# Optimization experiments

Hardware: AMD Instinct MI355X
Metric: run time of the kernel (lower is better)

The kernel has to match this reference:

```python
import jax, jax.numpy as jnp
import numpy as np
import math

L = 4      # model_layers
D = 512    # model_filters
H = 32     # heads = max(D//16, 1)
DH = D // H  # 16
S = 1024   # dataset_dimension == max_len == seq_len
B = 2
EPS = 1e-5


def setup_inputs() -> dict:
    key = jax.random.key(0)
    ks = jax.random.split(key, 12)
    scale = 0.02
    n = lambda k, shape: jax.random.normal(k, shape, dtype=jnp.float32) * scale
    return {
        "x": jax.random.normal(ks[0], (B, S), dtype=jnp.float32),
        "Winit": n(ks[1], (D,)),               # init_linear weight (1->D)
        "binit": jnp.zeros((D,), jnp.float32),
        "Wq": n(ks[2], (L, D, D)), "bq": jnp.zeros((L, D), jnp.float32),
        "Wk": n(ks[3], (L, D, D)), "bk": jnp.zeros((L, D), jnp.float32),
        "Wv": n(ks[4], (L, D, D)), "bv": jnp.zeros((L, D), jnp.float32),
        "Er": jax.random.normal(ks[5], (L, S, DH), dtype=jnp.float32) * scale,
        "Wlin": n(ks[6], (L, D, D)), "blin": jnp.zeros((L, D), jnp.float32),
        "ln_g": jnp.ones((L, D), jnp.float32), "ln_b": jnp.zeros((L, D), jnp.float32),
        "Wout": n(ks[7], (D, 1)),              # output_linear, no bias
    }


def layernorm(x, g, b):
    mu = jnp.mean(x, axis=-1, keepdims=True)
    var = jnp.mean(jnp.square(x - mu), axis=-1, keepdims=True)
    return (x - mu) * jax.lax.rsqrt(var + EPS) * g + b


def rel_attn(h, Wq, bq, Wk, bk, Wv, bv, Er):
    # h: [B, S, D]
    b_, s_, _ = h.shape
    q = (h @ Wq + bq).reshape(b_, s_, H, DH).transpose(0, 2, 1, 3)  # [B,H,S,dh]
    k = (h @ Wk + bk).reshape(b_, s_, H, DH).transpose(0, 2, 1, 3)
    v = (h @ Wv + bv).reshape(b_, s_, H, DH).transpose(0, 2, 1, 3)
    # relative-position term with skew trick (seq_len == max_len -> full Er)
    QEr = jnp.einsum('bhsd,td->bhst', q, Er)                  # [B,H,S,S]
    padded = jnp.pad(QEr, ((0, 0), (0, 0), (0, 0), (1, 0)))   # pad left of last dim
    Srel = padded.reshape(b_, H, s_ + 1, s_)[:, :, 1:, :]     # skew
    scores = (jnp.einsum('bhsd,bhtd->bhst', q, k) + Srel) / math.sqrt(DH)
    mask = jnp.tril(jnp.ones((s_, s_), dtype=bool))           # causal
    scores = jnp.where(mask, scores, -jnp.inf)
    p = jax.nn.softmax(scores, axis=-1)
    o = jnp.einsum('bhst,bhtd->bhsd', p, v)
    return o.transpose(0, 2, 1, 3).reshape(b_, s_, D)


def reference(x, Winit, binit, Wq, bq, Wk, bk, Wv, bv, Er, Wlin, blin, ln_g, ln_b, Wout):
    # init_linear(1->D) on scalar per position, then exact gelu
    h = jax.nn.gelu(x[..., None] * Winit + binit, approximate=False)  # [B,S,D]
    for l in range(L):
        a = rel_attn(h, Wq[l], bq[l], Wk[l], bk[l], Wv[l], bv[l], Er[l])
        y = layernorm(a @ Wlin[l] + blin[l], ln_g[l], ln_b[l])
        h = h + jax.nn.gelu(y, approximate=False)
    return h.sum(axis=-2) @ Wout  # [B,1]
```

## Files before the change

kernel.cpp:

```cpp
#include <hip/hip_runtime.h>
#include <math.h>

#define NL 4
#define DIM 512
#define NH 32
#define DHD 16
#define SEQ 1024
#define NB 2
#define LN_EPS 1e-5f
#define NEGF (-1e30f)
#define QSC 0.36067376022224085f

typedef _Float16 half4 __attribute__((ext_vector_type(4)));
typedef _Float16 half8 __attribute__((ext_vector_type(8)));
typedef float floatx4 __attribute__((ext_vector_type(4)));

__device__ __forceinline__ float gelu_exact(float x) {
    return 0.5f * x * (1.0f + erff(x * 0.70710678118654752f));
}

__device__ __forceinline__ void async16(const void* g, void* l) {
    __builtin_amdgcn_global_load_lds(
        (const __attribute__((address_space(1))) void*)g,
        (__attribute__((address_space(3))) void*)l, 16, 0, 0);
}

__global__ __launch_bounds__(256) void k_prep_all(const float* __restrict__ Wq,
        const float* __restrict__ Wk, const float* __restrict__ Wv,
        const float* __restrict__ Wlin, const float* __restrict__ bq,
        const float* __restrict__ bk, const float* __restrict__ bv,
        const float* __restrict__ Er, const float* __restrict__ x,
        const float* __restrict__ Wi, const float* __restrict__ bi,
        _Float16* __restrict__ Wqkvt, _Float16* __restrict__ Wlint,
        float* __restrict__ bqkv, _Float16* __restrict__ Erh,
        float* __restrict__ h, _Float16* __restrict__ hf) {
    __shared__ _Float16 lt[64][72];
    const int u = blockIdx.x;
    const int tid = threadIdx.x;
    if (u < 1024) {
        const int kx = u & 7, ny = (u >> 3) & 7, mz = u >> 6;
        const int l = mz >> 2, which = mz & 3;
        const float* src = (which == 0) ? Wq : (which == 1) ? Wk : (which == 2) ? Wv : Wlin;
        src += (size_t)l * 262144;
        const float scale = (which == 0) ? QSC : 1.0f;
        _Float16* dst = (which < 3) ? (Wqkvt + (size_t)l * 786432 + (size_t)which * 262144)
                                    : (Wlint + (size_t)l * 262144);
        const int k0 = kx << 6, n0 = ny << 6;
        #pragma unroll
        for (int p = 0; p < 4; p++) {
            int kl = (p << 4) + (tid >> 4);
            int n4 = (tid & 15) << 2;
            float4 wv = *(const float4*)(src + (size_t)(k0 + kl) * 512 + n0 + n4);
            lt[n4 + 0][kl] = (_Float16)(wv.x * scale);
            lt[n4 + 1][kl] = (_Float16)(wv.y * scale);
            lt[n4 + 2][kl] = (_Float16)(wv.z * scale);
            lt[n4 + 3][kl] = (_Float16)(wv.w * scale);
        }
        __syncthreads();
        int nl = tid >> 2, k16 = (tid & 3) << 4;
        float4* d4 = (float4*)(dst + (size_t)(n0 + nl) * 512 + k0 + k16);
        const float4* s4 = (const float4*)&lt[nl][k16];
        d4[0] = s4[0];
        d4[1] = s4[1];
    } else if (u < 2048) {
        int idx0 = ((u - 1024) << 10) + (tid << 2);
        int d = idx0 & 511, bs = idx0 >> 9;
        float xs = x[bs];
        float4 wv = *(const float4*)(Wi + d);
        float4 bv = *(const float4*)(bi + d);
        float4 r;
        r.x = gelu_exact(xs * wv.x + bv.x);
        r.y = gelu_exact(xs * wv.y + bv.y);
        r.z = gelu_exact(xs * wv.z + bv.z);
        r.w = gelu_exact(xs * wv.w + bv.w);
        *(float4*)(h + idx0) = r;
        half4 rh = {(_Float16)r.x, (_Float16)r.y, (_Float16)r.z, (_Float16)r.w};
        *(half4*)(hf + idx0) = rh;
    } else {
        int idx = ((u - 2048) << 8) + tid;
        if (idx < NL * 1536) {
            int l = idx / 1536, j = idx % 1536;
            int which = j >> 9, jj = j & 511;
            float val = (which == 0) ? bq[l * 512 + jj] * QSC
                      : (which == 1) ? bk[l * 512 + jj] : bv[l * 512 + jj];
            bqkv[idx] = val;
        }
        int e = idx - NL * 1536;
        if (e >= 0 && e < NL * SEQ * DHD) Erh[e] = (_Float16)Er[e];
    }
}

__global__ __launch_bounds__(256) void k_gemm_qkv(const _Float16* __restrict__ A,
        const _Float16* __restrict__ Bt, const float* __restrict__ bias,
        _Float16* __restrict__ o16) {
    __shared__ _Float16 As[2 * 64 * 32];
    __shared__ _Float16 Bs[2 * 128 * 32];
    const int tid = threadIdx.x;
    const int w = tid >> 6, lane = tid & 63;
    const int nn = lane & 15, qd = lane >> 4;
    const int wm = (w & 1) << 5, wn = (w >> 1) << 6;
    const int m0 = blockIdx.x << 6, n0 = blockIdx.y << 7;
    const int l2r = lane >> 2, l2c = (lane & 3) << 3;
    const _Float16* Ag = A + (size_t)(m0 + (w << 4) + l2r) * 512 + l2c;
    const _Float16* Bg = Bt + (size_t)(n0 + (w << 5) + l2r) * 512 + l2c;
    _Float16* Al = As + (w << 9);
    _Float16* Bl = Bs + (w << 10);
    floatx4 acc[2][4] = {};
    for (int k0 = 0; k0 < 512; k0 += 64) {
        __syncthreads();
        #pragma unroll
        for (int p = 0; p < 2; p++) {
            async16(Ag + k0 + (p << 5), Al + (p << 11));
            async16(Bg + k0 + (p << 5), Bl + (p << 12));
            async16(Bg + k0 + (p << 5) + (16 << 9), Bl + (p << 12) + (16 << 5));
        }
        __syncthreads();
        #pragma unroll
        for (int ks = 0; ks < 2; ks++) {
            half8 af[2], bf[4];
            #pragma unroll
            for (int t = 0; t < 2; t++)
                af[t] = *(const half8*)&As[(ks << 11) + ((wm + (t << 4) + nn) << 5) + (qd << 3)];
            #pragma unroll
            for (int t = 0; t < 4; t++)
                bf[t] = *(const half8*)&Bs[(ks << 12) + ((wn + (t << 4) + nn) << 5) + (qd << 3)];
            #pragma unroll
            for (int ti = 0; ti < 2; ti++)
                #pragma unroll
                for (int tj = 0; tj < 4; tj++)
                    acc[ti][tj] = __builtin_amdgcn_mfma_f32_16x16x32_f16(
                            af[ti], bf[tj], acc[ti][tj], 0, 0, 0);
        }
    }
    float bv4[4];
    #pragma unroll
    for (int tj = 0; tj < 4; tj++) bv4[tj] = bias[n0 + wn + (tj << 4) + nn];
    #pragma unroll
    for (int ti = 0; ti < 2; ti++) {
        int rowg = m0 + wm + (ti << 4) + (qd << 2);
        #pragma unroll
        for (int tj = 0; tj < 4; tj++) {
            int colg = n0 + wn + (tj << 4) + nn;
            int which = colg >> 9, ci = colg & 511;
            _Float16* op = o16 + (size_t)which * 1048576 + (size_t)rowg * 512 + ci;
            #pragma unroll
            for (int r = 0; r < 4; r++)
                op[(size_t)r * 512] = (_Float16)(acc[ti][tj][r] + bv4[tj]);
        }
    }
}

__global__ __launch_bounds__(256) void k_gemm_lin(const _Float16* __restrict__ A,
        const _Float16* __restrict__ Bt, const float* __restrict__ bias,
        float* __restrict__ y) {
    __shared__ _Float16 As[2 * 64 * 32];
    __shared__ _Float16 Bs[2 * 64 * 32];
    const int tid = threadIdx.x;
    const int w = tid >> 6, lane = tid & 63;
    const int nn = lane & 15, qd = lane >> 4;
    const int wm = (w & 1) << 5, wn = (w >> 1) << 5;
    const int m0 = blockIdx.x << 6, n0 = blockIdx.y << 6;
    const int l2r = lane >> 2, l2c = (lane & 3) << 3;
    const _Float16* Ag = A + (size_t)(m0 + (w << 4) + l2r) * 512 + l2c;
    const _Float16* Bg = Bt + (size_t)(n0 + (w << 4) + l2r) * 512 + l2c;
    _Float16* Al = As + (w << 9);
    _Float16* Bl = Bs + (w << 9);
    floatx4 acc[2][2] = {};
    for (int k0 = 0; k0 < 512; k0 += 64) {
        __syncthreads();
        #pragma unroll
        for (int p = 0; p < 2; p++) {
            async16(Ag + k0 + (p << 5), Al + (p << 11));
            async16(Bg + k0 + (p << 5), Bl + (p << 11));
        }
        __syncthreads();
        #pragma unroll
        for (int ks = 0; ks < 2; ks++) {
            half8 af[2], bf[2];
            #pragma unroll
            for (int t = 0; t < 2; t++) {
                af[t] = *(const half8*)&As[(ks << 11) + ((wm + (t << 4) + nn) << 5) + (qd << 3)];
                bf[t] = *(const half8*)&Bs[(ks << 11) + ((wn + (t << 4) + nn) << 5) + (qd << 3)];
            }
            #pragma unroll
            for (int ti = 0; ti < 2; ti++)
                #pragma unroll
                for (int tj = 0; tj < 2; tj++)
                    acc[ti][tj] = __builtin_amdgcn_mfma_f32_16x16x32_f16(
                            af[ti], bf[tj], acc[ti][tj], 0, 0, 0);
        }
    }
    float bv2[2];
    #pragma unroll
    for (int tj = 0; tj < 2; tj++) bv2[tj] = bias[n0 + wn + (tj << 4) + nn];
    #pragma unroll
    for (int ti = 0; ti < 2; ti++) {
        int rg = m0 + wm + (ti << 4) + (qd << 2);
        #pragma unroll
        for (int tj = 0; tj < 2; tj++) {
            int colg = n0 + wn + (tj << 4) + nn;
            float* op = y + (size_t)rg * 512 + colg;
            #pragma unroll
            for (int r = 0; r < 4; r++)
                op[(size_t)r * 512] = acc[ti][tj][r] + bv2[tj];
        }
    }
}

__global__ __launch_bounds__(256, 4) void k_attn_mfma(const _Float16* __restrict__ q,
        const _Float16* __restrict__ k, const _Float16* __restrict__ v,
        const _Float16* __restrict__ Er, _Float16* __restrict__ aout) {
    __shared__ _Float16 Ks[256][20];
    __shared__ _Float16 Vts[16][268];
    __shared__ float Rel[4][16][80];
    const int tid = threadIdx.x;
    const int wid = tid >> 6, lane = tid & 63;
    const int nn = lane & 15, a4 = (lane >> 4) << 2;
    const int b_ = blockIdx.x >> 5, h_ = blockIdx.x & 31;
    const int y = blockIdx.y;
    const int t_ = tid >> 2, c4 = (tid & 3) << 2;
    const int r0p[2] = {64 * y, 64 * (15 - y)};
    const int R = r0p[1] + 64;

    half4 qf[2];
    floatx4 O[2];
    float m[2], lsum[2];
    #pragma unroll
    for (int ph = 0; ph < 2; ph++) {
        int s0w = r0p[ph] + (wid << 4);
        qf[ph] = *(const half4*)(q + ((size_t)(b_ * SEQ + s0w + nn)) * DIM + h_ * DHD + a4);
        O[ph] = (floatx4){0.f, 0.f, 0.f, 0.f};
        m[ph] = NEGF;
        lsum[ph] = 0.f;
    }

    for (int part = 0; part < 4; part++) {
        const int p0 = part << 8;
        if (p0 >= R) break;
        const int pend = (R < p0 + 256) ? R : (p0 + 256);
        __syncthreads();
        const int ng = (pend - p0) >> 6;
        for (int g = 0; g < ng; g++) {
            int rl = (g << 6) + t_;
            size_t gb = ((size_t)(b_ * SEQ + p0 + rl)) * DIM + h_ * DHD + c4;
            *(half4*)&Ks[rl][c4] = *(const half4*)(k + gb);
            half4 vv4 = *(const half4*)(v + gb);
            Vts[c4 + 0][rl] = vv4.x;
            Vts[c4 + 1][rl] = vv4.y;
            Vts[c4 + 2][rl] = vv4.z;
            Vts[c4 + 3][rl] = vv4.w;
        }
        __syncthreads();
        #pragma unroll
        for (int ph = 0; ph < 2; ph++) {
            const int r0 = r0p[ph];
            const int s0w = r0 + (wid << 4);
            const int hi = (r0 + 64 < pend) ? (r0 + 64) : pend;
            for (int ct = p0; ct < hi; ct += 64) {
                const int ctl = ct - p0;
                const int jbw = 1008 - s0w + ct;
                #pragma unroll
                for (int jt = 0; jt < 5; jt++) {
                    int j = jbw + (jt << 4) + nn;
                    j = (j < SEQ - 1) ? j : (SEQ - 1);
                    half4 ef = *(const half4*)(Er + (size_t)j * DHD + a4);
                    floatx4 racc = {0.f, 0.f, 0.f, 0.f};
                    racc = __builtin_amdgcn_mfma_f32_16x16x16f16(ef, qf[ph], racc, 0, 0, 0);
                    *(floatx4*)&Rel[wid][nn][(jt << 4) + a4] = racc;
                }
                float st[4][4];
                const bool diag = (ct == r0);
                #pragma unroll
                for (int tt = 0; tt < 4; tt++) {
                    half4 kf = *(const half4*)&Ks[ctl + (tt << 4) + nn][a4];
                    floatx4 sacc = {0.f, 0.f, 0.f, 0.f};
                    sacc = __builtin_amdgcn_mfma_f32_16x16x16f16(kf, qf[ph], sacc, 0, 0, 0);
                    #pragma unroll
                    for (int r = 0; r < 4; r++) {
                        int tl = (tt << 4) + a4 + r;
                        float sv = sacc[r] + Rel[wid][nn][15 - nn + tl];
                        if (diag && (tl > (wid << 4) + nn)) sv = NEGF;
                        st[tt][r] = sv;
                    }
                }
                float cmax = NEGF;
                #pragma unroll
                for (int tt = 0; tt < 4; tt++)
                    #pragma unroll
                    for (int r = 0; r < 4; r++) cmax = fmaxf(cmax, st[tt][r]);
                cmax = fmaxf(cmax, __shfl_xor(cmax, 16));
                cmax = fmaxf(cmax, __shfl_xor(cmax, 32));
                float mnew = fmaxf(m[ph], cmax);
                float alpha = exp2f(m[ph] - mnew);
                m[ph] = mnew;
                float csum = 0.f;
                half4 pf[4];
                #pragma unroll
                for (int tt = 0; tt < 4; tt++) {
                    float p0e = exp2f(st[tt][0] - mnew);
                    float p1e = exp2f(st[tt][1] - mnew);
                    float p2e = exp2f(st[tt][2] - mnew);
                    float p3e = exp2f(st[tt][3] - mnew);
                    csum += (p0e + p1e) + (p2e + p3e);
                    half4 ph4 = {(_Float16)p0e, (_Float16)p1e, (_Float16)p2e, (_Float16)p3e};
                    pf[tt] = ph4;
                }
                lsum[ph] = lsum[ph] * alpha + csum;
                O[ph][0] *= alpha; O[ph][1] *= alpha; O[ph][2] *= alpha; O[ph][3] *= alpha;
                #pragma unroll
                for (int tt = 0; tt < 4; tt++) {
                    half4 vf = *(const half4*)&Vts[nn][ctl + (tt << 4) + a4];
                    O[ph] = __builtin_amdgcn_mfma_f32_16x16x16f16(vf, pf[tt], O[ph], 0, 0, 0);
                }
            }
        }
    }
    #pragma unroll
    for (int ph = 0; ph < 2; ph++) {
        float lt = lsum[ph];
        lt += __shfl_xor(lt, 16);
        lt += __shfl_xor(lt, 32);
        float linv = 1.0f / lt;
        int s0w = r0p[ph] + (wid << 4);
        half4 ov = { (_Float16)(O[ph][0] * linv), (_Float16)(O[ph][1] * linv),
                     (_Float16)(O[ph][2] * linv), (_Float16)(O[ph][3] * linv) };
        *(half4*)(aout + ((size_t)(b_ * SEQ + s0w + nn)) * DIM + h_ * DHD + a4) = ov;
    }
}

__global__ __launch_bounds__(256) void k_ln_gelu_res(const float* __restrict__ y,
        const float* __restrict__ gam, const float* __restrict__ bet,
        float* __restrict__ h, _Float16* __restrict__ hf) {
    int row = (blockIdx.x << 2) + (threadIdx.x >> 6);
    int lane = threadIdx.x & 63;
    const float* yr = y + (size_t)row * DIM + (lane << 3);
    float4 v0 = *(const float4*)(yr);
    float4 v1 = *(const float4*)(yr + 4);
    float sum = (v0.x + v0.y) + (v0.z + v0.w) + (v1.x + v1.y) + (v1.z + v1.w);
    float sq = v0.x*v0.x + v0.y*v0.y + v0.z*v0.z + v0.w*v0.w
             + v1.x*v1.x + v1.y*v1.y + v1.z*v1.z + v1.w*v1.w;
    #pragma unroll
    for (int off = 32; off > 0; off >>= 1) {
        sum += __shfl_xor(sum, off);
        sq  += __shfl_xor(sq, off);
    }
    float mu = sum * (1.0f / DIM);
    float var = sq * (1.0f / DIM) - mu * mu;
    float rs = rsqrtf(var + LN_EPS);
    float4 g0 = *(const float4*)(gam + (lane << 3));
    float4 g1 = *(const float4*)(gam + (lane << 3) + 4);
    float4 b0 = *(const float4*)(bet + (lane << 3));
    float4 b1 = *(const float4*)(bet + (lane << 3) + 4);
    float* hr = h + (size_t)row * DIM + (lane << 3);
    float4 h0 = *(const float4*)(hr);
    float4 h1 = *(const float4*)(hr + 4);
    float o[8];
    o[0] = h0.x + gelu_exact((v0.x - mu) * rs * g0.x + b0.x);
    o[1] = h0.y + gelu_exact((v0.y - mu) * rs * g0.y + b0.y);
    o[2] = h0.z + gelu_exact((v0.z - mu) * rs * g0.z + b0.z);
    o[3] = h0.w + gelu_exact((v0.w - mu) * rs * g0.w + b0.w);
    o[4] = h1.x + gelu_exact((v1.x - mu) * rs * g1.x + b1.x);
    o[5] = h1.y + gelu_exact((v1.y - mu) * rs * g1.y + b1.y);
    o[6] = h1.z + gelu_exact((v1.z - mu) * rs * g1.z + b1.z);
    o[7] = h1.w + gelu_exact((v1.w - mu) * rs * g1.w + b1.w);
    *(float4*)(hr)     = make_float4(o[0], o[1], o[2], o[3]);
    *(float4*)(hr + 4) = make_float4(o[4], o[5], o[6], o[7]);
    half8 oh = {(_Float16)o[0], (_Float16)o[1], (_Float16)o[2], (_Float16)o[3],
                (_Float16)o[4], (_Float16)o[5], (_Float16)o[6], (_Float16)o[7]};
    *(half8*)(hf + (size_t)row * DIM + (lane << 3)) = oh;
}

__global__ __launch_bounds__(256) void k_colsum(const float* __restrict__ h,
        float* __restrict__ partial) {
    int bt = blockIdx.x;
    int b_ = bt >> 4, t = bt & 15;
    int tid = threadIdx.x;
    #pragma unroll
    for (int half = 0; half < 2; half++) {
        int d = half * 256 + tid;
        float acc = 0.f;
        for (int i = 0; i < 64; i++)
            acc += h[((size_t)(b_ * SEQ + t * 64 + i)) * DIM + d];
        partial[(size_t)bt * DIM + d] = acc;
    }
}

__global__ __launch_bounds__(256) void k_final(const float* __restrict__ partial,
        const float* __restrict__ Wout, float* __restrict__ out) {
    __shared__ float red[4][2];
    int tid = threadIdx.x;
    float acc0 = 0.f, acc1 = 0.f;
    #pragma unroll
    for (int half = 0; half < 2; half++) {
        int d = half * 256 + tid;
        float w = Wout[d];
        float s0 = 0.f, s1 = 0.f;
        for (int t = 0; t < 16; t++) {
            s0 += partial[t * DIM + d];
            s1 += partial[(16 + t) * DIM + d];
        }
        acc0 += s0 * w;
        acc1 += s1 * w;
    }
    #pragma unroll
    for (int off = 32; off > 0; off >>= 1) {
        acc0 += __shfl_down(acc0, off);
        acc1 += __shfl_down(acc1, off);
    }
    if ((tid & 63) == 0) { red[tid >> 6][0] = acc0; red[tid >> 6][1] = acc1; }
    __syncthreads();
    if (tid == 0) {
        out[0] = red[0][0] + red[1][0] + red[2][0] + red[3][0];
        out[1] = red[0][1] + red[1][1] + red[2][1] + red[3][1];
    }
}

extern "C" void kernel_launch(void* const* d_in, const int* in_sizes, int n_in,
                              void* d_out, int out_size, void* d_ws, size_t ws_size,
                              hipStream_t stream) {
    const float* x    = (const float*)d_in[0];
    const float* Wi   = (const float*)d_in[1];
    const float* bi   = (const float*)d_in[2];
    const float* Wq   = (const float*)d_in[3];
    const float* bq   = (const float*)d_in[4];
    const float* Wk   = (const float*)d_in[5];
    const float* bk   = (const float*)d_in[6];
    const float* Wv   = (const float*)d_in[7];
    const float* bv   = (const float*)d_in[8];
    const float* Er   = (const float*)d_in[9];
    const float* Wlin = (const float*)d_in[10];
    const float* blin = (const float*)d_in[11];
    const float* lng  = (const float*)d_in[12];
    const float* lnb  = (const float*)d_in[13];
    const float* Wout = (const float*)d_in[14];
    float* out = (float*)d_out;

    float* ws = (float*)d_ws;
    const size_t N1 = 1048576;
    float*     h     = ws;
    _Float16*  hf    = (_Float16*)(ws + N1);
    _Float16*  qh    = (_Float16*)(ws + N1 + N1/2);
    _Float16*  ah    = (_Float16*)(ws + 3 * N1);
    float*     y     = ws + 3 * N1 + N1/2;
    _Float16*  Wqkvt = (_Float16*)(ws + 4 * N1 + N1/2);
    _Float16*  Wlint = (_Float16*)(ws + 6 * N1);
    float*     bqkv  = ws + 6 * N1 + N1/2;
    _Float16*  Erh   = (_Float16*)(ws + 6 * N1 + N1/2 + 8192);
    float*     pa    = ws + 6 * N1 + N1/2 + 8192 + 32768;

    k_prep_all<<<dim3(2328), dim3(256), 0, stream>>>(Wq, Wk, Wv, Wlin, bq, bk, bv,
            Er, x, Wi, bi, Wqkvt, Wlint, bqkv, Erh, h, hf);
    for (int l = 0; l < NL; l++) {
        k_gemm_qkv<<<dim3(32, 12), dim3(256), 0, stream>>>(
                hf, Wqkvt + (size_t)l * 786432, bqkv + l * 1536, qh);
        k_attn_mfma<<<dim3(NB * NH, 8), dim3(256), 0, stream>>>(
                qh, qh + 1048576, qh + 2097152, Erh + (size_t)l * 16384, ah);
        k_gemm_lin<<<dim3(32, 8), dim3(256), 0, stream>>>(
                ah, Wlint + (size_t)l * 262144, blin + l * 512, y);
        k_ln_gelu_res<<<dim3(512), dim3(256), 0, stream>>>(
                y, lng + l * 512, lnb + l * 512, h, hf);
    }
    k_colsum<<<dim3(32), dim3(256), 0, stream>>>(h, pa);
    k_final<<<dim3(1), dim3(256), 0, stream>>>(pa, Wout, out);
}
```

Baseline: 315.0 us.

## Split attention into one row tile per block and shrink QKV GEMM tiles

The attention kernel no longer pairs a low and a high 64-row tile per block to balance causal work. Each block now handles one 64-row query tile, so the grid grows to 16 tiles per head and gets more parallelism and fewer live registers, at the cost of uneven per-block work. The QKV GEMM now reuses the 64x64-tile linear GEMM as a template, doubling its grid to 768 blocks at the cost of reloading each A tile more often.

```diff
diff --git a/kernel.cpp b/kernel.cpp
--- a/kernel.cpp
+++ b/kernel.cpp
@@ -90,69 +90,10 @@
     }
 }
 
-__global__ __launch_bounds__(256) void k_gemm_qkv(const _Float16* __restrict__ A,
+template<int F16OUT>
+__global__ __launch_bounds__(256) void k_gemm(const _Float16* __restrict__ A,
         const _Float16* __restrict__ Bt, const float* __restrict__ bias,
-        _Float16* __restrict__ o16) {
-    __shared__ _Float16 As[2 * 64 * 32];
-    __shared__ _Float16 Bs[2 * 128 * 32];
-    const int tid = threadIdx.x;
-    const int w = tid >> 6, lane = tid & 63;
-    const int nn = lane & 15, qd = lane >> 4;
-    const int wm = (w & 1) << 5, wn = (w >> 1) << 6;
-    const int m0 = blockIdx.x << 6, n0 = blockIdx.y << 7;
-    const int l2r = lane >> 2, l2c = (lane & 3) << 3;
-    const _Float16* Ag = A + (size_t)(m0 + (w << 4) + l2r) * 512 + l2c;
-    const _Float16* Bg = Bt + (size_t)(n0 + (w << 5) + l2r) * 512 + l2c;
-    _Float16* Al = As + (w << 9);
-    _Float16* Bl = Bs + (w << 10);
-    floatx4 acc[2][4] = {};
-    for (int k0 = 0; k0 < 512; k0 += 64) {
-        __syncthreads();
-        #pragma unroll
-        for (int p = 0; p < 2; p++) {
-            async16(Ag + k0 + (p << 5), Al + (p << 11));
-            async16(Bg + k0 + (p << 5), Bl + (p << 12));
-            async16(Bg + k0 + (p << 5) + (16 << 9), Bl + (p << 12) + (16 << 5));
-        }
-        __syncthreads();
-        #pragma unroll
-        for (int ks = 0; ks < 2; ks++) {
-            half8 af[2], bf[4];
-            #pragma unroll
-            for (int t = 0; t < 2; t++)
-                af[t] = *(const half8*)&As[(ks << 11) + ((wm + (t << 4) + nn) << 5) + (qd << 3)];
-            #pragma unroll
-            for (int t = 0; t < 4; t++)
-                bf[t] = *(const half8*)&Bs[(ks << 12) + ((wn + (t << 4) + nn) << 5) + (qd << 3)];
-            #pragma unroll
-            for (int ti = 0; ti < 2; ti++)
-                #pragma unroll
-                for (int tj = 0; tj < 4; tj++)
-                    acc[ti][tj] = __builtin_amdgcn_mfma_f32_16x16x32_f16(
-                            af[ti], bf[tj], acc[ti][tj], 0, 0, 0);
-        }
-    }
-    float bv4[4];
-    #pragma unroll
-    for (int tj = 0; tj < 4; tj++) bv4[tj] = bias[n0 + wn + (tj << 4) + nn];
-    #pragma unroll
-    for (int ti = 0; ti < 2; ti++) {
-        int rowg = m0 + wm + (ti << 4) + (qd << 2);
-        #pragma unroll
-        for (int tj = 0; tj < 4; tj++) {
-            int colg = n0 + wn + (tj << 4) + nn;
-            int which = colg >> 9, ci = colg & 511;
-            _Float16* op = o16 + (size_t)which * 1048576 + (size_t)rowg * 512 + ci;
-            #pragma unroll
-            for (int r = 0; r < 4; r++)
-                op[(size_t)r * 512] = (_Float16)(acc[ti][tj][r] + bv4[tj]);
-        }
-    }
-}
-
-__global__ __launch_bounds__(256) void k_gemm_lin(const _Float16* __restrict__ A,
-        const _Float16* __restrict__ Bt, const float* __restrict__ bias,
-        float* __restrict__ y) {
+        _Float16* __restrict__ o16, float* __restrict__ o32) {
     __shared__ _Float16 As[2 * 64 * 32];
     __shared__ _Float16 Bs[2 * 64 * 32];
     const int tid = threadIdx.x;
@@ -199,10 +140,18 @@
         #pragma unroll
         for (int tj = 0; tj < 2; tj++) {
             int colg = n0 + wn + (tj << 4) + nn;
-            float* op = y + (size_t)rg * 512 + colg;
-            #pragma unroll
-            for (int r = 0; r < 4; r++)
-                op[(size_t)r * 512] = acc[ti][tj][r] + bv2[tj];
+            if (F16OUT) {
+                int which = colg >> 9, ci = colg & 511;
+                _Float16* op = o16 + (size_t)which * 1048576 + (size_t)rg * 512 + ci;
+                #pragma unroll
+                for (int r = 0; r < 4; r++)
+                    op[(size_t)r * 512] = (_Float16)(acc[ti][tj][r] + bv2[tj]);
+            } else {
+                float* op = o32 + (size_t)rg * 512 + colg;
+                #pragma unroll
+                for (int r = 0; r < 4; r++)
+                    op[(size_t)r * 512] = acc[ti][tj][r] + bv2[tj];
+            }
         }
     }
 }
@@ -219,20 +168,13 @@
     const int b_ = blockIdx.x >> 5, h_ = blockIdx.x & 31;
     const int y = blockIdx.y;
     const int t_ = tid >> 2, c4 = (tid & 3) << 2;
-    const int r0p[2] = {64 * y, 64 * (15 - y)};
-    const int R = r0p[1] + 64;
-
-    half4 qf[2];
-    floatx4 O[2];
-    float m[2], lsum[2];
-    #pragma unroll
-    for (int ph = 0; ph < 2; ph++) {
-        int s0w = r0p[ph] + (wid << 4);
-        qf[ph] = *(const half4*)(q + ((size_t)(b_ * SEQ + s0w + nn)) * DIM + h_ * DHD + a4);
-        O[ph] = (floatx4){0.f, 0.f, 0.f, 0.f};
-        m[ph] = NEGF;
-        lsum[ph] = 0.f;
-    }
+    const int r0 = y << 6;
+    const int s0w = r0 + (wid << 4);
+    const int R = r0 + 64;
+
+    half4 qf = *(const half4*)(q + ((size_t)(b_ * SEQ + s0w + nn)) * DIM + h_ * DHD + a4);
+    floatx4 O = {0.f, 0.f, 0.f, 0.f};
+    float m = NEGF, lsum = 0.f;
 
     for (int part = 0; part < 4; part++) {
         const int p0 = part << 8;
@@ -251,81 +193,71 @@
             Vts[c4 + 3][rl] = vv4.w;
         }
         __syncthreads();
-        #pragma unroll
-        for (int ph = 0; ph < 2; ph++) {
-            const int r0 = r0p[ph];
-            const int s0w = r0 + (wid << 4);
-            const int hi = (r0 + 64 < pend) ? (r0 + 64) : pend;
-            for (int ct = p0; ct < hi; ct += 64) {
-                const int ctl = ct - p0;
-                const int jbw = 1008 - s0w + ct;
-                #pragma unroll
-                for (int jt = 0; jt < 5; jt++) {
-                    int j = jbw + (jt << 4) + nn;
-                    j = (j < SEQ - 1) ? j : (SEQ - 1);
-                    half4 ef = *(const half4*)(Er + (size_t)j * DHD + a4);
-                    floatx4 racc = {0.f, 0.f, 0.f, 0.f};
-                    racc = __builtin_amdgcn_mfma_f32_16x16x16f16(ef, qf[ph], racc, 0, 0, 0);
-                    *(floatx4*)&Rel[wid][nn][(jt << 4) + a4] = racc;
+        for (int ct = p0; ct < pend; ct += 64) {
+            const int ctl = ct - p0;
+            const int jbw = 1008 - s0w + ct;
+            #pragma unroll
+            for (int jt = 0; jt < 5; jt++) {
+                int j = jbw + (jt << 4) + nn;
+                j = (j < SEQ - 1) ? j : (SEQ - 1);
+                half4 ef = *(const half4*)(Er + (size_t)j * DHD + a4);
+                floatx4 racc = {0.f, 0.f, 0.f, 0.f};
+                racc = __builtin_amdgcn_mfma_f32_16x16x16f16(ef, qf, racc, 0, 0, 0);
+                *(floatx4*)&Rel[wid][nn][(jt << 4) + a4] = racc;
+            }
+            float st[4][4];
+            const bool diag = (ct == r0);
+            #pragma unroll
+            for (int tt = 0; tt < 4; tt++) {
+                half4 kf = *(const half4*)&Ks[ctl + (tt << 4) + nn][a4];
+                floatx4 sacc = {0.f, 0.f, 0.f, 0.f};
+                sacc = __builtin_amdgcn_mfma_f32_16x16x16f16(kf, qf, sacc, 0, 0, 0);
+                #pragma unroll
+                for (int r = 0; r < 4; r++) {
+                    int tl = (tt << 4) + a4 + r;
+                    float sv = sacc[r] + Rel[wid][nn][15 - nn + tl];
+                    if (diag && (tl > (wid << 4) + nn)) sv = NEGF;
+                    st[tt][r] = sv;
                 }
-                float st[4][4];
-                const bool diag = (ct == r0);
-                #pragma unroll
-                for (int tt = 0; tt < 4; tt++) {
-                    half4 kf = *(const half4*)&Ks[ctl + (tt << 4) + nn][a4];
-                    floatx4 sacc = {0.f, 0.f, 0.f, 0.f};
-                    sacc = __builtin_amdgcn_mfma_f32_16x16x16f16(kf, qf[ph], sacc, 0, 0, 0);
-                    #pragma unroll
-                    for (int r = 0; r < 4; r++) {
-                        int tl = (tt << 4) + a4 + r;
-                        float sv = sacc[r] + Rel[wid][nn][15 - nn + tl];
-                        if (diag && (tl > (wid << 4) + nn)) sv = NEGF;
-                        st[tt][r] = sv;
-                    }
-                }
-                float cmax = NEGF;
-                #pragma unroll
-                for (int tt = 0; tt < 4; tt++)
-                    #pragma unroll
-                    for (int r = 0; r < 4; r++) cmax = fmaxf(cmax, st[tt][r]);
-                cmax = fmaxf(cmax, __shfl_xor(cmax, 16));
-                cmax = fmaxf(cmax, __shfl_xor(cmax, 32));
-                float mnew = fmaxf(m[ph], cmax);
-                float alpha = exp2f(m[ph] - mnew);
-                m[ph] = mnew;
-                float csum = 0.f;
-                half4 pf[4];
-                #pragma unroll
-                for (int tt = 0; tt < 4; tt++) {
-                    float p0e = exp2f(st[tt][0] - mnew);
-                    float p1e = exp2f(st[tt][1] - mnew);
-                    float p2e = exp2f(st[tt][2] - mnew);
-                    float p3e = exp2f(st[tt][3] - mnew);
-                    csum += (p0e + p1e) + (p2e + p3e);
-                    half4 ph4 = {(_Float16)p0e, (_Float16)p1e, (_Float16)p2e, (_Float16)p3e};
-                    pf[tt] = ph4;
-                }
-                lsum[ph] = lsum[ph] * alpha + csum;
-                O[ph][0] *= alpha; O[ph][1] *= alpha; O[ph][2] *= alpha; O[ph][3] *= alpha;
-                #pragma unroll
-                for (int tt = 0; tt < 4; tt++) {
-                    half4 vf = *(const half4*)&Vts[nn][ctl + (tt << 4) + a4];
-                    O[ph] = __builtin_amdgcn_mfma_f32_16x16x16f16(vf, pf[tt], O[ph], 0, 0, 0);
-                }
-            }
-        }
-    }
-    #pragma unroll
-    for (int ph = 0; ph < 2; ph++) {
-        float lt = lsum[ph];
-        lt += __shfl_xor(lt, 16);
-        lt += __shfl_xor(lt, 32);
-        float linv = 1.0f / lt;
-        int s0w = r0p[ph] + (wid << 4);
-        half4 ov = { (_Float16)(O[ph][0] * linv), (_Float16)(O[ph][1] * linv),
-                     (_Float16)(O[ph][2] * linv), (_Float16)(O[ph][3] * linv) };
-        *(half4*)(aout + ((size_t)(b_ * SEQ + s0w + nn)) * DIM + h_ * DHD + a4) = ov;
-    }
+            }
+            float cmax = NEGF;
+            #pragma unroll
+            for (int tt = 0; tt < 4; tt++)
+                #pragma unroll
+                for (int r = 0; r < 4; r++) cmax = fmaxf(cmax, st[tt][r]);
+            cmax = fmaxf(cmax, __shfl_xor(cmax, 16));
+            cmax = fmaxf(cmax, __shfl_xor(cmax, 32));
+            float mnew = fmaxf(m, cmax);
+            float alpha = exp2f(m - mnew);
+            m = mnew;
+            float csum = 0.f;
+            half4 pf[4];
+            #pragma unroll
+            for (int tt = 0; tt < 4; tt++) {
+                float p0e = exp2f(st[tt][0] - mnew);
+                float p1e = exp2f(st[tt][1] - mnew);
+                float p2e = exp2f(st[tt][2] - mnew);
+                float p3e = exp2f(st[tt][3] - mnew);
+                csum += (p0e + p1e) + (p2e + p3e);
+                half4 ph4 = {(_Float16)p0e, (_Float16)p1e, (_Float16)p2e, (_Float16)p3e};
+                pf[tt] = ph4;
+            }
+            lsum = lsum * alpha + csum;
+            O[0] *= alpha; O[1] *= alpha; O[2] *= alpha; O[3] *= alpha;
+            #pragma unroll
+            for (int tt = 0; tt < 4; tt++) {
+                half4 vf = *(const half4*)&Vts[nn][ctl + (tt << 4) + a4];
+                O = __builtin_amdgcn_mfma_f32_16x16x16f16(vf, pf[tt], O, 0, 0, 0);
+            }
+        }
+    }
+    float lt = lsum;
+    lt += __shfl_xor(lt, 16);
+    lt += __shfl_xor(lt, 32);
+    float linv = 1.0f / lt;
+    half4 ov = { (_Float16)(O[0] * linv), (_Float16)(O[1] * linv),
+                 (_Float16)(O[2] * linv), (_Float16)(O[3] * linv) };
+    *(half4*)(aout + ((size_t)(b_ * SEQ + s0w + nn)) * DIM + h_ * DHD + a4) = ov;
 }
 
 __global__ __launch_bounds__(256) void k_ln_gelu_res(const float* __restrict__ y,
@@ -451,12 +383,12 @@
     k_prep_all<<<dim3(2328), dim3(256), 0, stream>>>(Wq, Wk, Wv, Wlin, bq, bk, bv,
             Er, x, Wi, bi, Wqkvt, Wlint, bqkv, Erh, h, hf);
     for (int l = 0; l < NL; l++) {
-        k_gemm_qkv<<<dim3(32, 12), dim3(256), 0, stream>>>(
-                hf, Wqkvt + (size_t)l * 786432, bqkv + l * 1536, qh);
-        k_attn_mfma<<<dim3(NB * NH, 8), dim3(256), 0, stream>>>(
+        k_gemm<1><<<dim3(32, 24), dim3(256), 0, stream>>>(
+                hf, Wqkvt + (size_t)l * 786432, bqkv + l * 1536, qh, nullptr);
+        k_attn_mfma<<<dim3(NB * NH, 16), dim3(256), 0, stream>>>(
                 qh, qh + 1048576, qh + 2097152, Erh + (size_t)l * 16384, ah);
-        k_gemm_lin<<<dim3(32, 8), dim3(256), 0, stream>>>(
-                ah, Wlint + (size_t)l * 262144, blin + l * 512, y);
+        k_gemm<0><<<dim3(32, 8), dim3(256), 0, stream>>>(
+                ah, Wlint + (size_t)l * 262144, blin + l * 512, nullptr, y);
         k_ln_gelu_res<<<dim3(512), dim3(256), 0, stream>>>(
                 y, lng + l * 512, lnb + l * 512, h, hf);
     }
```

New measurement: 325.7 us. +3.4%, slower.
